# Kernel tuning notes

Measured on AMD Instinct MI355X. Metric: run time of the kernel, lower is better.

The kernel has to match this reference:

```python
import jax, jax.numpy as jnp
import numpy as np

H, DH = 16, 64          # num_heads, dim_head
DIM = 1024              # dim_ltn
EPS = 1e-5


def setup_inputs() -> dict:
    key = jax.random.key(0)
    ks = jax.random.split(key, 8)
    b, n_txt, t, m = 2, 2048, 4, 256
    text = jax.random.normal(ks[0], (b, n_txt, DIM), dtype=jnp.float32)
    image = jax.random.normal(ks[1], (b, t, m, DIM), dtype=jnp.float32)
    locations = jax.random.randint(ks[2], (b, n_txt), 0, 2)  # 0/1 media markers
    s = DIM ** -0.5
    Wq = jax.random.normal(ks[3], (DIM, H * DH), dtype=jnp.float32) * s
    Wkv = jax.random.normal(ks[4], (DIM, 2 * H * DH), dtype=jnp.float32) * s
    Wo = jax.random.normal(ks[5], (H * DH, DIM), dtype=jnp.float32) * s
    ln_gamma = jnp.ones((DIM,), dtype=jnp.float32)
    ln_beta = jnp.zeros((DIM,), dtype=jnp.float32)
    return {"text": text, "image": image, "locations": locations,
            "Wq": Wq, "Wkv": Wkv, "Wo": Wo,
            "ln_gamma": ln_gamma, "ln_beta": ln_beta}


def reference(text, image, locations, Wq, Wkv, Wo, ln_gamma, ln_beta):
    scale = DH ** -0.5
    b, t, m, d = image.shape
    # LayerNorm(text)
    mu = text.mean(-1, keepdims=True)
    var = ((text - mu) ** 2).mean(-1, keepdims=True)
    tn = (text - mu) / jnp.sqrt(var + EPS) * ln_gamma + ln_beta
    img = image.reshape(b, t * m, d)             # b (t m) d
    q = tn @ Wq                                  # b n (h dh)
    k, v = jnp.split(img @ Wkv, 2, axis=-1)      # each b tm (h dh)
    split_heads = lambda x: x.reshape(x.shape[0], x.shape[1], H, DH).transpose(0, 2, 1, 3)
    q, k, v = split_heads(q), split_heads(k), split_heads(v)
    attn = jnp.einsum('bhid,bhjd->bhij', q, k) * scale   # b h n (t m)
    txt_time = jnp.cumsum(locations, axis=-1)            # b n : media index per text token
    viz_time = jnp.repeat(jnp.arange(1, t + 1), m)       # (t m)
    # only_attend_to_immediate -> equality mask
    mask = txt_time[:, None, :, None] == viz_time[None, None, None, :]
    neg = -jnp.finfo(attn.dtype).max
    attn = jnp.where(mask, attn, neg)
    attn = jax.nn.softmax(attn, axis=-1)
    # zero attention for text tokens before any media (txt_time == 0)
    attn = jnp.where((txt_time == 0)[:, None, :, None], 0.0, attn)
    out = jnp.einsum('bhij,bhjd->bhid', attn, v)
    out = out.transpose(0, 2, 1, 3).reshape(b, -1, H * DH)
    return out @ Wo
```

## Files before the change

kernel.cpp:

```cpp
#include <hip/hip_runtime.h>

#define BATCH 2
#define NTXT  2048
#define TMED  4
#define MMED  256
#define TM    (TMED * MMED)
#define DIM   1024
#define NH    16
#define DHD   64
#define KVW   2048
#define RMAX  256
#define RT    32

typedef _Float16 f16x8 __attribute__((ext_vector_type(8)));
typedef float    f32x4 __attribute__((ext_vector_type(4)));

__global__ __launch_bounds__(1024) void k1_scan_cvt_tr(
    const int* __restrict__ loc, const float* __restrict__ image,
    const float* __restrict__ Wkv, int* __restrict__ tt, int* __restrict__ seg,
    float* __restrict__ ipart, _Float16* __restrict__ img16,
    _Float16* __restrict__ WkvT) {
  __shared__ int buf[NTXT];
  __shared__ float tile[64][65];
  __shared__ int wmin[2][16];
  const int idx = blockIdx.x;
  const int tid = threadIdx.x;
  if (idx < BATCH) {
    const int b = idx;
    buf[tid]        = loc[b * NTXT + tid];
    buf[tid + 1024] = loc[b * NTXT + tid + 1024];
    __syncthreads();
    for (int off = 1; off < NTXT; off <<= 1) {
      int a0 = (tid >= off) ? buf[tid - off] : 0;
      int a1 = buf[tid + 1024 - off];
      __syncthreads();
      buf[tid] += a0;
      buf[tid + 1024] += a1;
      __syncthreads();
    }
    const int v0 = buf[tid], v1 = buf[tid + 1024];
    tt[b * NTXT + tid]        = v0;
    tt[b * NTXT + tid + 1024] = v1;
    const int lane = tid & 63, w = tid >> 6;
    const unsigned long long b1a = __ballot(v0 >= 1);
    const unsigned long long b1b = __ballot(v1 >= 1);
    const unsigned long long b5a = __ballot(v0 >= 5);
    const unsigned long long b5b = __ballot(v1 >= 5);
    if (lane == 0) {
      int s1 = NTXT, s5 = NTXT;
      if (b1a)      s1 = w * 64 + (__ffsll(b1a) - 1);
      else if (b1b) s1 = 1024 + w * 64 + (__ffsll(b1b) - 1);
      if (b5a)      s5 = w * 64 + (__ffsll(b5a) - 1);
      else if (b5b) s5 = 1024 + w * 64 + (__ffsll(b5b) - 1);
      wmin[0][w] = s1;
      wmin[1][w] = s5;
    }
    __syncthreads();
    if (tid == 0) {
      int s = NTXT, e = NTXT;
#pragma unroll
      for (int i = 0; i < 16; i++) {
        s = min(s, wmin[0][i]);
        e = min(e, wmin[1][i]);
      }
      seg[b * 2]     = s;
      seg[b * 2 + 1] = e - s;
    }
  } else if (idx < BATCH + 256) {
    const int j = idx - BATCH;
    const int b = j >> 7, rt = j & 127;
    const size_t base = (size_t)(b * TM + rt * 8) * DIM + tid;
    const float* p = image + base;
    _Float16* q = img16 + base;
    float s = 0.f;
#pragma unroll
    for (int r = 0; r < 8; r++) {
      const float v = p[(size_t)r * DIM];
      s += v;
      q[(size_t)r * DIM] = (_Float16)v;
    }
    ipart[(size_t)(b * 128 + rt) * DIM + tid] = s;
  } else {
    const int j2 = idx - BATCH - 256;
    const int k0 = (j2 & 15) * 64, n0 = (j2 >> 4) * 64;
    const int r = tid >> 4, c4 = (tid & 15) * 4;
    const float4 v = *reinterpret_cast<const float4*>(
        Wkv + (size_t)(k0 + r) * KVW + n0 + c4);
    tile[r][c4 + 0] = v.x; tile[r][c4 + 1] = v.y;
    tile[r][c4 + 2] = v.z; tile[r][c4 + 3] = v.w;
    __syncthreads();
    if (tid < 512) {
      const int n = tid >> 3, kc = (tid & 7) * 8;
      f16x8 h;
#pragma unroll
      for (int u = 0; u < 8; u++) h[u] = (_Float16)tile[kc + u][n];
      *reinterpret_cast<f16x8*>(WkvT + (size_t)(n0 + n) * DIM + k0 + kc) = h;
    }
  }
}

__global__ __launch_bounds__(256) void k2_prep(
    const float* __restrict__ Wkv, const float* __restrict__ text,
    const float* __restrict__ gamma, const float* __restrict__ beta,
    const int* __restrict__ seg, const float* __restrict__ ipart,
    float* __restrict__ tn, float* __restrict__ vbar) {
  __shared__ float red[256];
  const int idx = blockIdx.x;
  const int tid = threadIdx.x;
  if (idx < 64) {
    const int b = idx >> 5, rt = idx & 31;
    const int i0 = seg[b * 2];
    const int cnt = min(seg[b * 2 + 1], RMAX);
    for (int r = rt; r < cnt; r += RT) {
      const float* xrow = text + (size_t)(b * NTXT + i0 + r) * DIM;
      float x[4];
      float s = 0.f;
#pragma unroll
      for (int u = 0; u < 4; u++) { x[u] = xrow[tid + 256 * u]; s += x[u]; }
      red[tid] = s; __syncthreads();
      for (int st = 128; st > 0; st >>= 1) {
        if (tid < st) red[tid] += red[tid + st];
        __syncthreads();
      }
      const float mu = red[0] * (1.0f / DIM); __syncthreads();
      float vs = 0.f;
#pragma unroll
      for (int u = 0; u < 4; u++) { float d = x[u] - mu; vs += d * d; }
      red[tid] = vs; __syncthreads();
      for (int st = 128; st > 0; st >>= 1) {
        if (tid < st) red[tid] += red[tid + st];
        __syncthreads();
      }
      const float rstd = rsqrtf(red[0] * (1.0f / DIM) + 1e-5f); __syncthreads();
      float* trow = tn + (size_t)(b * RMAX + r) * DIM;
#pragma unroll
      for (int u = 0; u < 4; u++) {
        const int c = tid + 256 * u;
        trow[c] = (x[u] - mu) * rstd * gamma[c] + beta[c];
      }
      __syncthreads();
    }
  } else {
    const int j = idx - 64;
    const int b = j >> 5, et = (j >> 3) & 3, cc = j & 7;
    const int e = et * 256 + tid;
    const int c0 = cc * 128;
    if (tid < 128) {
      float s = 0.f;
      for (int p = 0; p < 128; p++)
        s += ipart[(size_t)(b * 128 + p) * DIM + c0 + tid];
      red[tid] = s * (1.0f / (float)TM);
    }
    __syncthreads();
    float s = 0.f;
    for (int c = 0; c < 128; c++)
      s += red[c] * Wkv[(size_t)(c0 + c) * KVW + DIM + e];
    atomicAdd(&vbar[b * DIM + e], s);
  }
}

__global__ __launch_bounds__(512) void k3_gemm_qproj_obar(
    const _Float16* __restrict__ img16, const _Float16* __restrict__ WkvT,
    const float* __restrict__ Wq, const float* __restrict__ Wo,
    const float* __restrict__ tn, const float* __restrict__ vbar,
    const int* __restrict__ seg, _Float16* __restrict__ kv16,
    float* __restrict__ qbuf, float* __restrict__ obar) {
  __shared__ __align__(16) char smem[16384];
  const int idx = blockIdx.x;
  const int tid = threadIdx.x;
  if (idx < 256) {
    _Float16* As = (_Float16*)smem;
    _Float16* Bs = As + 128 * 32;
    const int lane = tid & 63, wid = tid >> 6;
    const int wm = wid & 3, wn = wid >> 2;
    const int row0 = (idx >> 4) * 128, col0 = (idx & 15) * 128;
    const int srow = tid >> 2, skc = (tid & 3) * 8;
    const int frow = lane & 15, fq = lane >> 4;
    f32x4 acc[2][4] = {};
    for (int k0 = 0; k0 < DIM; k0 += 32) {
      const f16x8 av = *reinterpret_cast<const f16x8*>(
          img16 + (size_t)(row0 + srow) * DIM + k0 + skc);
      const f16x8 bv = *reinterpret_cast<const f16x8*>(
          WkvT + (size_t)(col0 + srow) * DIM + k0 + skc);
      __syncthreads();
      *reinterpret_cast<f16x8*>(As + tid * 8) = av;
      *reinterpret_cast<f16x8*>(Bs + tid * 8) = bv;
      __syncthreads();
      f16x8 af[2], bf[4];
#pragma unroll
      for (int mt = 0; mt < 2; mt++)
        af[mt] = *reinterpret_cast<const f16x8*>(
            As + (wm * 32 + mt * 16 + frow) * 32 + fq * 8);
#pragma unroll
      for (int nt = 0; nt < 4; nt++)
        bf[nt] = *reinterpret_cast<const f16x8*>(
            Bs + (wn * 64 + nt * 16 + frow) * 32 + fq * 8);
#pragma unroll
      for (int mt = 0; mt < 2; mt++)
#pragma unroll
        for (int nt = 0; nt < 4; nt++)
          acc[mt][nt] = __builtin_amdgcn_mfma_f32_16x16x32_f16(
              af[mt], bf[nt], acc[mt][nt], 0, 0, 0);
    }
#pragma unroll
    for (int mt = 0; mt < 2; mt++)
#pragma unroll
      for (int nt = 0; nt < 4; nt++) {
        const int col = col0 + wn * 64 + nt * 16 + frow;
#pragma unroll
        for (int r = 0; r < 4; r++) {
          const int row = row0 + wm * 32 + mt * 16 + fq * 4 + r;
          kv16[(size_t)row * KVW + col] = (_Float16)acc[mt][nt][r];
        }
      }
  } else if (idx < 320) {
    float* tn_s = (float*)smem;
    const int j = idx - 256;
    const int b = j >> 5, nt = (j >> 2) & 7, cc = j & 3;
    const int n0 = nt * 128, c0 = cc * 256;
    const int n = tid & 127, cs = tid >> 7;
    const int cnt = min(seg[b * 2 + 1], RMAX);
    for (int r0 = 0; r0 < cnt; r0 += 8) {
      const int rows = min(8, cnt - r0);
      for (int i = tid; i < 8 * 256; i += 512) {
        const int r = i >> 8, c = i & 255;
        tn_s[i] = (r < rows) ? tn[(size_t)(b * RMAX + r0 + r) * DIM + c0 + c]
                             : 0.f;
      }
      __syncthreads();
      float acc[8] = {};
      for (int ci = 0; ci < 64; ci++) {
        const int c = cs * 64 + ci;
        const float w = Wq[(size_t)(c0 + c) * DIM + n0 + n];
#pragma unroll
        for (int rr = 0; rr < 8; rr++) acc[rr] += tn_s[rr * 256 + c] * w;
      }
      for (int rr = 0; rr < rows; rr++)
        atomicAdd(&qbuf[(size_t)(b * RMAX + r0 + rr) * DIM + n0 + n], acc[rr]);
      __syncthreads();
    }
  } else {
    float* vb_s = (float*)smem;
    const int j = idx - 320;
    const int b = j >> 4, et = (j >> 3) & 1, cc = j & 7;
    const int e = et * 512 + tid;
    const int c0 = cc * 128;
    if (tid < 128) vb_s[tid] = vbar[b * DIM + c0 + tid];
    __syncthreads();
    float s = 0.f;
    for (int c = 0; c < 128; c++)
      s += vb_s[c] * Wo[(size_t)(c0 + c) * DIM + e];
    atomicAdd(&obar[b * DIM + e], s);
  }
}

__global__ __launch_bounds__(256) void k4_fill_attn(
    const float* __restrict__ text, const _Float16* __restrict__ kv16,
    const float* __restrict__ Wq, const float* __restrict__ Wo,
    const float* __restrict__ gamma, const float* __restrict__ beta,
    const int* __restrict__ tt, const int* __restrict__ seg,
    const float* __restrict__ obar, const float* __restrict__ qbuf,
    float* __restrict__ oacc, float* __restrict__ out) {
  __shared__ float red[256];
  __shared__ float pbuf[256];
  const int idx = blockIdx.x;
  const int tid = threadIdx.x;
  if (idx < BATCH * NTXT) {
    const int b = idx >> 11;
    const int i = idx & (NTXT - 1);
    const int t = tt[b * NTXT + i];
    float* orow = out + (size_t)(b * NTXT + i) * DIM;
    if (t == 0) {
      for (int c = tid; c < DIM; c += 256) orow[c] = 0.f;
      return;
    }
    if (t > TMED) {
      const float* ob = obar + b * DIM;
      for (int c = tid; c < DIM; c += 256) orow[c] = ob[c];
      return;
    }
    if (i - seg[b * 2] < RMAX) return;
    __shared__ float tns[DIM];
    __shared__ float qrow[DIM];
    __shared__ float oaccs[DIM];
    const float* xrow = text + (size_t)(b * NTXT + i) * DIM;
    float x[4];
    float s = 0.f;
#pragma unroll
    for (int u = 0; u < 4; u++) { x[u] = xrow[tid + 256 * u]; s += x[u]; }
    red[tid] = s; __syncthreads();
    for (int st = 128; st > 0; st >>= 1) {
      if (tid < st) red[tid] += red[tid + st];
      __syncthreads();
    }
    const float mu = red[0] * (1.0f / DIM); __syncthreads();
    float vs = 0.f;
#pragma unroll
    for (int u = 0; u < 4; u++) { float d = x[u] - mu; vs += d * d; }
    red[tid] = vs; __syncthreads();
    for (int st = 128; st > 0; st >>= 1) {
      if (tid < st) red[tid] += red[tid + st];
      __syncthreads();
    }
    const float rstd = rsqrtf(red[0] * (1.0f / DIM) + 1e-5f); __syncthreads();
#pragma unroll
    for (int u = 0; u < 4; u++) {
      const int c = tid + 256 * u;
      tns[c] = (x[u] - mu) * rstd * gamma[c] + beta[c];
    }
    __syncthreads();
    {
      float qa[4] = {0.f, 0.f, 0.f, 0.f};
      for (int c = 0; c < DIM; c++) {
        const float tv = tns[c];
        const float* w = Wq + (size_t)c * DIM + tid;
#pragma unroll
        for (int u = 0; u < 4; u++) qa[u] += tv * w[256 * u];
      }
#pragma unroll
      for (int u = 0; u < 4; u++) qrow[tid + 256 * u] = qa[u];
    }
    __syncthreads();
    const size_t kvrow0 = (size_t)(b * TM + (t - 1) * MMED) * KVW;
    const int d0 = tid & 63, g = tid >> 6;
    for (int h = 0; h < NH; h++) {
      const _Float16* krow = kv16 + kvrow0 + (size_t)tid * KVW + h * DHD;
      float sc = 0.f;
#pragma unroll
      for (int d = 0; d < DHD; d++) sc += qrow[h * DHD + d] * (float)krow[d];
      sc *= 0.125f;
      red[tid] = sc; __syncthreads();
      for (int st = 128; st > 0; st >>= 1) {
        if (tid < st) red[tid] = fmaxf(red[tid], red[tid + st]);
        __syncthreads();
      }
      const float mx = red[0]; __syncthreads();
      const float e = __expf(sc - mx);
      red[tid] = e; __syncthreads();
      for (int st = 128; st > 0; st >>= 1) {
        if (tid < st) red[tid] += red[tid + st];
        __syncthreads();
      }
      const float inv = 1.0f / red[0]; __syncthreads();
      pbuf[tid] = e * inv; __syncthreads();
      const _Float16* vbase = kv16 + kvrow0 + (size_t)(g * 64) * KVW + DIM + h * DHD + d0;
      float a = 0.f;
#pragma unroll 8
      for (int jj = 0; jj < 64; jj++) a += pbuf[g * 64 + jj] * (float)vbase[(size_t)jj * KVW];
      red[tid] = a; __syncthreads();
      if (tid < 64)
        oaccs[h * DHD + tid] = red[tid] + red[64 + tid] + red[128 + tid] + red[192 + tid];
      __syncthreads();
    }
    float oa[4] = {0.f, 0.f, 0.f, 0.f};
    for (int c = 0; c < DIM; c++) {
      const float ov = oaccs[c];
      const float* w = Wo + (size_t)c * DIM + tid;
#pragma unroll
      for (int u = 0; u < 4; u++) oa[u] += ov * w[256 * u];
    }
#pragma unroll
    for (int u = 0; u < 4; u++) orow[tid + 256 * u] = oa[u];
  } else {
    __shared__ float qs[DHD];
    const int j = idx - BATCH * NTXT;
    const int h = j & 15, rt = (j >> 4) & 31, b = j >> 9;
    const int i0 = seg[b * 2];
    const int cnt = min(seg[b * 2 + 1], RMAX);
    const int d0 = tid & 63, g = tid >> 6;
    for (int r = rt; r < cnt; r += RT) {
      const int i = i0 + r;
      const int t = tt[b * NTXT + i];
      if (tid < 64) qs[tid] = qbuf[(size_t)(b * RMAX + r) * DIM + h * DHD + tid];
      __syncthreads();
      const size_t kvrow0 = (size_t)(b * TM + (t - 1) * MMED) * KVW;
      const _Float16* krow = kv16 + kvrow0 + (size_t)tid * KVW + h * DHD;
      float sc = 0.f;
#pragma unroll
      for (int d = 0; d < DHD; d += 8) {
        const f16x8 kk = *reinterpret_cast<const f16x8*>(krow + d);
#pragma unroll
        for (int u = 0; u < 8; u++) sc += qs[d + u] * (float)kk[u];
      }
      sc *= 0.125f;
      red[tid] = sc; __syncthreads();
      for (int st = 128; st > 0; st >>= 1) {
        if (tid < st) red[tid] = fmaxf(red[tid], red[tid + st]);
        __syncthreads();
      }
      const float mx = red[0]; __syncthreads();
      const float e = __expf(sc - mx);
      red[tid] = e; __syncthreads();
      for (int st = 128; st > 0; st >>= 1) {
        if (tid < st) red[tid] += red[tid + st];
        __syncthreads();
      }
      const float inv = 1.0f / red[0]; __syncthreads();
      pbuf[tid] = e * inv; __syncthreads();
      const _Float16* vbase = kv16 + kvrow0 + (size_t)(g * 64) * KVW + DIM + h * DHD + d0;
      float a = 0.f;
#pragma unroll 8
      for (int jj = 0; jj < 64; jj++) a += pbuf[g * 64 + jj] * (float)vbase[(size_t)jj * KVW];
      red[tid] = a; __syncthreads();
      if (tid < 64)
        oacc[(size_t)(b * RMAX + r) * DIM + h * DHD + tid] =
            red[tid] + red[64 + tid] + red[128 + tid] + red[192 + tid];
      __syncthreads();
    }
  }
}

__global__ __launch_bounds__(256) void k5_oproj(
    const float* __restrict__ oacc, const float* __restrict__ Wo,
    const int* __restrict__ seg, float* __restrict__ out) {
  const int ct = blockIdx.x;
  const int rt = blockIdx.y;
  const int b = blockIdx.z;
  const int i0 = seg[b * 2];
  const int cnt = min(seg[b * 2 + 1], RMAX);
  const int tid = threadIdx.x;
  const int d0 = tid & 63, g = tid >> 6;
  __shared__ float op[4][64];
  for (int r = rt; r < cnt; r += RT) {
    const float* arow = oacc + (size_t)(b * RMAX + r) * DIM;
    const float* wo = Wo + (size_t)(g * 256) * DIM + ct * 64 + d0;
    float s = 0.f;
    for (int c = 0; c < 256; c++) s += arow[g * 256 + c] * wo[(size_t)c * DIM];
    op[g][d0] = s; __syncthreads();
    if (tid < 64)
      out[(size_t)(b * NTXT + i0 + r) * DIM + ct * 64 + tid] =
          op[0][tid] + op[1][tid] + op[2][tid] + op[3][tid];
    __syncthreads();
  }
}

extern "C" void kernel_launch(void* const* d_in, const int* in_sizes, int n_in,
                              void* d_out, int out_size, void* d_ws, size_t ws_size,
                              hipStream_t stream) {
  const float* text  = (const float*)d_in[0];
  const float* image = (const float*)d_in[1];
  const int*   loc   = (const int*)d_in[2];
  const float* Wq    = (const float*)d_in[3];
  const float* Wkv   = (const float*)d_in[4];
  const float* Wo    = (const float*)d_in[5];
  const float* gamma = (const float*)d_in[6];
  const float* beta  = (const float*)d_in[7];
  float* out = (float*)d_out;

  _Float16* kv16  = (_Float16*)d_ws;
  _Float16* WkvT  = kv16 + (size_t)BATCH * TM * KVW;
  float*    oacc  = (float*)WkvT;
  _Float16* img16 = WkvT + (size_t)KVW * DIM;
  float*    tn    = (float*)(img16 + (size_t)BATCH * TM * DIM);
  float*    qbuf  = tn + (size_t)BATCH * RMAX * DIM;
  float*    vbar  = qbuf + (size_t)BATCH * RMAX * DIM;
  float*    obar  = vbar + BATCH * DIM;
  int*      tt    = (int*)(obar + BATCH * DIM);
  int*      seg   = tt + BATCH * NTXT;
  float*    ipart = (float*)(seg + 8);

  hipMemsetAsync(qbuf, 0,
                 ((size_t)BATCH * RMAX * DIM + 2 * BATCH * DIM) * sizeof(float),
                 stream);
  k1_scan_cvt_tr<<<BATCH + 256 + 512, 1024, 0, stream>>>(
      loc, image, Wkv, tt, seg, ipart, img16, WkvT);
  k2_prep<<<128, 256, 0, stream>>>(Wkv, text, gamma, beta, seg, ipart, tn, vbar);
  k3_gemm_qproj_obar<<<352, 512, 0, stream>>>(img16, WkvT, Wq, Wo, tn, vbar,
                                              seg, kv16, qbuf, obar);
  k4_fill_attn<<<BATCH * NTXT + NH * RT * BATCH, 256, 0, stream>>>(
      text, kv16, Wq, Wo, gamma, beta, tt, seg, obar, qbuf, oacc, out);
  k5_oproj<<<dim3(16, RT, BATCH), 256, 0, stream>>>(oacc, Wo, seg, out);
}
```

Baseline: 153.0 us.

## Fuse output projection into attention, register-prefetch GEMM, shuffle-based scan, in-kernel zeroing

Several changes land together. The block scan of media markers now uses wavefront shuffles instead of a shared-memory Hillis-Steele loop. The hipMemsetAsync is replaced by extra zeroing blocks in k1, and k2 zeroes the out rows of the segment. The KV GEMM now uses a K-tile of 64 with an XOR-swizzled LDS layout and register prefetch of the next tile. The separate k5 output projection is removed, and each attention block multiplies its head slice by Wo and atomically adds into out. The goal is fewer launches and better GEMM overlap, at the cost of many float atomics on out and nondeterministic summation order.

```diff
diff --git a/kernel.cpp b/kernel.cpp
--- a/kernel.cpp
+++ b/kernel.cpp
@@ -19,41 +19,50 @@
     const int* __restrict__ loc, const float* __restrict__ image,
     const float* __restrict__ Wkv, int* __restrict__ tt, int* __restrict__ seg,
     float* __restrict__ ipart, _Float16* __restrict__ img16,
-    _Float16* __restrict__ WkvT) {
-  __shared__ int buf[NTXT];
+    _Float16* __restrict__ WkvT, float* __restrict__ zbase) {
   __shared__ float tile[64][65];
+  __shared__ int wtot[16];
   __shared__ int wmin[2][16];
   const int idx = blockIdx.x;
   const int tid = threadIdx.x;
   if (idx < BATCH) {
     const int b = idx;
-    buf[tid]        = loc[b * NTXT + tid];
-    buf[tid + 1024] = loc[b * NTXT + tid + 1024];
-    __syncthreads();
-    for (int off = 1; off < NTXT; off <<= 1) {
-      int a0 = (tid >= off) ? buf[tid - off] : 0;
-      int a1 = buf[tid + 1024 - off];
-      __syncthreads();
-      buf[tid] += a0;
-      buf[tid + 1024] += a1;
-      __syncthreads();
-    }
-    const int v0 = buf[tid], v1 = buf[tid + 1024];
-    tt[b * NTXT + tid]        = v0;
-    tt[b * NTXT + tid + 1024] = v1;
     const int lane = tid & 63, w = tid >> 6;
-    const unsigned long long b1a = __ballot(v0 >= 1);
-    const unsigned long long b1b = __ballot(v1 >= 1);
-    const unsigned long long b5a = __ballot(v0 >= 5);
-    const unsigned long long b5b = __ballot(v1 >= 5);
-    if (lane == 0) {
-      int s1 = NTXT, s5 = NTXT;
-      if (b1a)      s1 = w * 64 + (__ffsll(b1a) - 1);
-      else if (b1b) s1 = 1024 + w * 64 + (__ffsll(b1b) - 1);
-      if (b5a)      s5 = w * 64 + (__ffsll(b5a) - 1);
-      else if (b5b) s5 = 1024 + w * 64 + (__ffsll(b5b) - 1);
-      wmin[0][w] = s1;
-      wmin[1][w] = s5;
+    const int e0 = tid * 2;
+    const int a0 = loc[b * NTXT + e0], a1 = loc[b * NTXT + e0 + 1];
+    const int p = a0 + a1;
+    int incl = p;
+#pragma unroll
+    for (int off = 1; off < 64; off <<= 1) {
+      const int t2 = __shfl_up(incl, off, 64);
+      if (lane >= off) incl += t2;
+    }
+    if (lane == 63) wtot[w] = incl;
+    __syncthreads();
+    if (tid < 16) {
+      const int v = wtot[tid];
+      int inc2 = v;
+#pragma unroll
+      for (int off = 1; off < 16; off <<= 1) {
+        const int t3 = __shfl_up(inc2, off, 64);
+        if (tid >= off) inc2 += t3;
+      }
+      wtot[tid] = inc2 - v;
+    }
+    __syncthreads();
+    const int base = wtot[w] + (incl - p);
+    const int t0v = base + a0, t1v = t0v + a1;
+    tt[b * NTXT + e0]     = t0v;
+    tt[b * NTXT + e0 + 1] = t1v;
+    {
+      const int c1 = (t1v >= 1) ? ((t0v >= 1) ? e0 : e0 + 1) : NTXT;
+      const int c5 = (t1v >= 5) ? ((t0v >= 5) ? e0 : e0 + 1) : NTXT;
+      const unsigned long long b1 = __ballot(t1v >= 1);
+      const unsigned long long b5 = __ballot(t1v >= 5);
+      int m1 = NTXT, m5 = NTXT;
+      if (b1) m1 = __shfl(c1, __ffsll(b1) - 1, 64);
+      if (b5) m5 = __shfl(c5, __ffsll(b5) - 1, 64);
+      if (lane == 0) { wmin[0][w] = m1; wmin[1][w] = m5; }
     }
     __syncthreads();
     if (tid == 0) {
@@ -80,7 +89,7 @@
       q[(size_t)r * DIM] = (_Float16)v;
     }
     ipart[(size_t)(b * 128 + rt) * DIM + tid] = s;
-  } else {
+  } else if (idx < BATCH + 256 + 512) {
     const int j2 = idx - BATCH - 256;
     const int k0 = (j2 & 15) * 64, n0 = (j2 >> 4) * 64;
     const int r = tid >> 4, c4 = (tid & 15) * 4;
@@ -96,6 +105,11 @@
       for (int u = 0; u < 8; u++) h[u] = (_Float16)tile[kc + u][n];
       *reinterpret_cast<f16x8*>(WkvT + (size_t)(n0 + n) * DIM + k0 + kc) = h;
     }
+  } else {
+    const int j = idx - (BATCH + 256 + 512);
+    float4* z = reinterpret_cast<float4*>(zbase);
+    const float4 zv = {0.f, 0.f, 0.f, 0.f};
+    for (int i = j * 1024 + tid; i < 132096; i += 16 * 1024) z[i] = zv;
   }
 }
 
@@ -103,7 +117,8 @@
     const float* __restrict__ Wkv, const float* __restrict__ text,
     const float* __restrict__ gamma, const float* __restrict__ beta,
     const int* __restrict__ seg, const float* __restrict__ ipart,
-    float* __restrict__ tn, float* __restrict__ vbar) {
+    float* __restrict__ tn, float* __restrict__ vbar,
+    float* __restrict__ out) {
   __shared__ float red[256];
   const int idx = blockIdx.x;
   const int tid = threadIdx.x;
@@ -140,7 +155,7 @@
       }
       __syncthreads();
     }
-  } else {
+  } else if (idx < 128) {
     const int j = idx - 64;
     const int b = j >> 5, et = (j >> 3) & 3, cc = j & 7;
     const int e = et * 256 + tid;
@@ -156,6 +171,14 @@
     for (int c = 0; c < 128; c++)
       s += red[c] * Wkv[(size_t)(c0 + c) * KVW + DIM + e];
     atomicAdd(&vbar[b * DIM + e], s);
+  } else {
+    const int b = idx - 128;
+    const int i0 = seg[b * 2];
+    const int cnt = min(seg[b * 2 + 1], RMAX);
+    for (int r = 0; r < cnt; r++) {
+      float* orow = out + (size_t)(b * NTXT + i0 + r) * DIM;
+      for (int c = tid; c < DIM; c += 256) orow[c] = 0.f;
+    }
   }
 }
 
@@ -165,42 +188,68 @@
     const float* __restrict__ tn, const float* __restrict__ vbar,
     const int* __restrict__ seg, _Float16* __restrict__ kv16,
     float* __restrict__ qbuf, float* __restrict__ obar) {
-  __shared__ __align__(16) char smem[16384];
+  __shared__ __align__(16) char smem[32768];
   const int idx = blockIdx.x;
   const int tid = threadIdx.x;
   if (idx < 256) {
     _Float16* As = (_Float16*)smem;
-    _Float16* Bs = As + 128 * 32;
+    _Float16* Bs = As + 128 * 64;
     const int lane = tid & 63, wid = tid >> 6;
     const int wm = wid & 3, wn = wid >> 2;
     const int row0 = (idx >> 4) * 128, col0 = (idx & 15) * 128;
-    const int srow = tid >> 2, skc = (tid & 3) * 8;
+    const int srow = tid >> 3, skc = (tid & 7) * 8;
     const int frow = lane & 15, fq = lane >> 4;
+    const int swk = skc ^ ((srow & 7) << 3);
     f32x4 acc[2][4] = {};
-    for (int k0 = 0; k0 < DIM; k0 += 32) {
-      const f16x8 av = *reinterpret_cast<const f16x8*>(
-          img16 + (size_t)(row0 + srow) * DIM + k0 + skc);
-      const f16x8 bv = *reinterpret_cast<const f16x8*>(
-          WkvT + (size_t)(col0 + srow) * DIM + k0 + skc);
-      __syncthreads();
-      *reinterpret_cast<f16x8*>(As + tid * 8) = av;
-      *reinterpret_cast<f16x8*>(Bs + tid * 8) = bv;
-      __syncthreads();
-      f16x8 af[2], bf[4];
-#pragma unroll
-      for (int mt = 0; mt < 2; mt++)
-        af[mt] = *reinterpret_cast<const f16x8*>(
-            As + (wm * 32 + mt * 16 + frow) * 32 + fq * 8);
-#pragma unroll
-      for (int nt = 0; nt < 4; nt++)
-        bf[nt] = *reinterpret_cast<const f16x8*>(
-            Bs + (wn * 64 + nt * 16 + frow) * 32 + fq * 8);
-#pragma unroll
-      for (int mt = 0; mt < 2; mt++)
-#pragma unroll
-        for (int nt = 0; nt < 4; nt++)
-          acc[mt][nt] = __builtin_amdgcn_mfma_f32_16x16x32_f16(
-              af[mt], bf[nt], acc[mt][nt], 0, 0, 0);
+    f16x8 a0v = *reinterpret_cast<const f16x8*>(
+        img16 + (size_t)(row0 + srow) * DIM + skc);
+    f16x8 a1v = *reinterpret_cast<const f16x8*>(
+        img16 + (size_t)(row0 + srow + 64) * DIM + skc);
+    f16x8 b0v = *reinterpret_cast<const f16x8*>(
+        WkvT + (size_t)(col0 + srow) * DIM + skc);
+    f16x8 b1v = *reinterpret_cast<const f16x8*>(
+        WkvT + (size_t)(col0 + srow + 64) * DIM + skc);
+    for (int k0 = 0; k0 < DIM; k0 += 64) {
+      __syncthreads();
+      *reinterpret_cast<f16x8*>(As + srow * 64 + swk)        = a0v;
+      *reinterpret_cast<f16x8*>(As + (srow + 64) * 64 + swk) = a1v;
+      *reinterpret_cast<f16x8*>(Bs + srow * 64 + swk)        = b0v;
+      *reinterpret_cast<f16x8*>(Bs + (srow + 64) * 64 + swk) = b1v;
+      __syncthreads();
+      if (k0 + 64 < DIM) {
+        a0v = *reinterpret_cast<const f16x8*>(
+            img16 + (size_t)(row0 + srow) * DIM + k0 + 64 + skc);
+        a1v = *reinterpret_cast<const f16x8*>(
+            img16 + (size_t)(row0 + srow + 64) * DIM + k0 + 64 + skc);
+        b0v = *reinterpret_cast<const f16x8*>(
+            WkvT + (size_t)(col0 + srow) * DIM + k0 + 64 + skc);
+        b1v = *reinterpret_cast<const f16x8*>(
+            WkvT + (size_t)(col0 + srow + 64) * DIM + k0 + 64 + skc);
+      }
+      f16x8 af[2][2], bf[2][4];
+#pragma unroll
+      for (int kk = 0; kk < 2; kk++) {
+#pragma unroll
+        for (int mt = 0; mt < 2; mt++) {
+          const int r = wm * 32 + mt * 16 + frow;
+          af[kk][mt] = *reinterpret_cast<const f16x8*>(
+              As + r * 64 + ((kk * 32 + fq * 8) ^ ((r & 7) << 3)));
+        }
+#pragma unroll
+        for (int nt = 0; nt < 4; nt++) {
+          const int c = wn * 64 + nt * 16 + frow;
+          bf[kk][nt] = *reinterpret_cast<const f16x8*>(
+              Bs + c * 64 + ((kk * 32 + fq * 8) ^ ((c & 7) << 3)));
+        }
+      }
+#pragma unroll
+      for (int kk = 0; kk < 2; kk++)
+#pragma unroll
+        for (int mt = 0; mt < 2; mt++)
+#pragma unroll
+          for (int nt = 0; nt < 4; nt++)
+            acc[mt][nt] = __builtin_amdgcn_mfma_f32_16x16x32_f16(
+                af[kk][mt], bf[kk][nt], acc[mt][nt], 0, 0, 0);
     }
 #pragma unroll
     for (int mt = 0; mt < 2; mt++)
@@ -260,7 +309,7 @@
     const float* __restrict__ gamma, const float* __restrict__ beta,
     const int* __restrict__ tt, const int* __restrict__ seg,
     const float* __restrict__ obar, const float* __restrict__ qbuf,
-    float* __restrict__ oacc, float* __restrict__ out) {
+    float* __restrict__ out) {
   __shared__ float red[256];
   __shared__ float pbuf[256];
   const int idx = blockIdx.x;
@@ -363,6 +412,7 @@
     for (int u = 0; u < 4; u++) orow[tid + 256 * u] = oa[u];
   } else {
     __shared__ float qs[DHD];
+    __shared__ float osl[DHD];
     const int j = idx - BATCH * NTXT;
     const int h = j & 15, rt = (j >> 4) & 31, b = j >> 9;
     const int i0 = seg[b * 2];
@@ -403,34 +453,20 @@
       for (int jj = 0; jj < 64; jj++) a += pbuf[g * 64 + jj] * (float)vbase[(size_t)jj * KVW];
       red[tid] = a; __syncthreads();
       if (tid < 64)
-        oacc[(size_t)(b * RMAX + r) * DIM + h * DHD + tid] =
-            red[tid] + red[64 + tid] + red[128 + tid] + red[192 + tid];
-      __syncthreads();
-    }
-  }
-}
-
-__global__ __launch_bounds__(256) void k5_oproj(
-    const float* __restrict__ oacc, const float* __restrict__ Wo,
-    const int* __restrict__ seg, float* __restrict__ out) {
-  const int ct = blockIdx.x;
-  const int rt = blockIdx.y;
-  const int b = blockIdx.z;
-  const int i0 = seg[b * 2];
-  const int cnt = min(seg[b * 2 + 1], RMAX);
-  const int tid = threadIdx.x;
-  const int d0 = tid & 63, g = tid >> 6;
-  __shared__ float op[4][64];
-  for (int r = rt; r < cnt; r += RT) {
-    const float* arow = oacc + (size_t)(b * RMAX + r) * DIM;
-    const float* wo = Wo + (size_t)(g * 256) * DIM + ct * 64 + d0;
-    float s = 0.f;
-    for (int c = 0; c < 256; c++) s += arow[g * 256 + c] * wo[(size_t)c * DIM];
-    op[g][d0] = s; __syncthreads();
-    if (tid < 64)
-      out[(size_t)(b * NTXT + i0 + r) * DIM + ct * 64 + tid] =
-          op[0][tid] + op[1][tid] + op[2][tid] + op[3][tid];
-    __syncthreads();
+        osl[tid] = red[tid] + red[64 + tid] + red[128 + tid] + red[192 + tid];
+      __syncthreads();
+      float* orow = out + (size_t)(b * NTXT + i) * DIM;
+#pragma unroll
+      for (int u = 0; u < 4; u++) {
+        const int c = tid + 256 * u;
+        const float* w = Wo + (size_t)(h * DHD) * DIM + c;
+        float s2 = 0.f;
+#pragma unroll 8
+        for (int d = 0; d < DHD; d++) s2 += osl[d] * w[(size_t)d * DIM];
+        atomicAdd(&orow[c], s2);
+      }
+      __syncthreads();
+    }
   }
 }
 
@@ -449,7 +485,6 @@
 
   _Float16* kv16  = (_Float16*)d_ws;
   _Float16* WkvT  = kv16 + (size_t)BATCH * TM * KVW;
-  float*    oacc  = (float*)WkvT;
   _Float16* img16 = WkvT + (size_t)KVW * DIM;
   float*    tn    = (float*)(img16 + (size_t)BATCH * TM * DIM);
   float*    qbuf  = tn + (size_t)BATCH * RMAX * DIM;
@@ -459,15 +494,12 @@
   int*      seg   = tt + BATCH * NTXT;
   float*    ipart = (float*)(seg + 8);
 
-  hipMemsetAsync(qbuf, 0,
-                 ((size_t)BATCH * RMAX * DIM + 2 * BATCH * DIM) * sizeof(float),
-                 stream);
-  k1_scan_cvt_tr<<<BATCH + 256 + 512, 1024, 0, stream>>>(
-      loc, image, Wkv, tt, seg, ipart, img16, WkvT);
-  k2_prep<<<128, 256, 0, stream>>>(Wkv, text, gamma, beta, seg, ipart, tn, vbar);
+  k1_scan_cvt_tr<<<BATCH + 256 + 512 + 16, 1024, 0, stream>>>(
+      loc, image, Wkv, tt, seg, ipart, img16, WkvT, qbuf);
+  k2_prep<<<130, 256, 0, stream>>>(Wkv, text, gamma, beta, seg, ipart,
+                                   tn, vbar, out);
   k3_gemm_qproj_obar<<<352, 512, 0, stream>>>(img16, WkvT, Wq, Wo, tn, vbar,
                                               seg, kv16, qbuf, obar);
   k4_fill_attn<<<BATCH * NTXT + NH * RT * BATCH, 256, 0, stream>>>(
-      text, kv16, Wq, Wo, gamma, beta, tt, seg, obar, qbuf, oacc, out);
-  k5_oproj<<<dim3(16, RT, BATCH), 256, 0, stream>>>(oacc, Wo, seg, out);
+      text, kv16, Wq, Wo, gamma, beta, tt, seg, obar, qbuf, out);
 }
```

Result: no change. 152.8 us, median of 2 (-0.1%).
